# Performance work log

Hardware: AMD Instinct MI355X
Metric: run time of the kernel (lower is better)

Reference implementation:

```python
import jax, jax.numpy as jnp
import numpy as np

N_NODES = 50000
N_EDGES = 800000
IN_DIM = 64
EDGE_DIM = 16
HID = 128
L = 3
G = 128  # number of graphs in the batch
EPS = 1e-5


def _glorot(key, shape):
    fan_in, fan_out = shape[0], shape[1]
    lim = float(np.sqrt(6.0 / (fan_in + fan_out)))
    return jax.random.uniform(key, shape, jnp.float32, -lim, lim)


def setup_inputs() -> dict:
    key = jax.random.key(0)
    ks = jax.random.split(key, 40)
    inp = {}
    inp["x"] = jax.random.uniform(ks[0], (N_NODES, IN_DIM), jnp.float32)
    inp["edge_index"] = jax.random.randint(ks[1], (2, N_EDGES), 0, N_NODES, jnp.int64)
    inp["edge_attr"] = jax.random.normal(ks[2], (N_EDGES, EDGE_DIM), jnp.float32)
    inp["batch"] = jnp.sort(jax.random.randint(ks[3], (N_NODES,), 0, G, jnp.int64))
    # ligand / protein input MLPs: Linear-ReLU-Linear-ReLU
    inp["lig_w1"] = _glorot(ks[4], (IN_DIM, HID)); inp["lig_b1"] = jnp.zeros((HID,), jnp.float32)
    inp["lig_w2"] = _glorot(ks[5], (HID, HID));    inp["lig_b2"] = jnp.zeros((HID,), jnp.float32)
    inp["prot_w1"] = _glorot(ks[6], (IN_DIM, HID)); inp["prot_b1"] = jnp.zeros((HID,), jnp.float32)
    inp["prot_w2"] = _glorot(ks[7], (HID, HID));    inp["prot_b2"] = jnp.zeros((HID,), jnp.float32)
    # per-layer GINEConv params (stacked over layers)
    inp["edge_w"] = jnp.stack([_glorot(ks[8 + i], (EDGE_DIM, HID)) for i in range(L)])
    inp["edge_b"] = jnp.zeros((L, HID), jnp.float32)
    inp["nn_w1"] = jnp.stack([_glorot(ks[12 + i], (HID, HID)) for i in range(L)])
    inp["nn_b1"] = jnp.zeros((L, HID), jnp.float32)
    inp["nn_w2"] = jnp.stack([_glorot(ks[16 + i], (HID, HID)) for i in range(L)])
    inp["nn_b2"] = jnp.zeros((L, HID), jnp.float32)
    # GraphNorm params: weight=1, bias=0, mean_scale=1
    inp["gn_w"] = jnp.ones((L, HID), jnp.float32)
    inp["gn_b"] = jnp.zeros((L, HID), jnp.float32)
    inp["gn_ms"] = jnp.ones((L, HID), jnp.float32)
    # output head: Linear-ReLU-Linear(1)
    inp["fc_w1"] = _glorot(ks[20], (HID, HID)); inp["fc_b1"] = jnp.zeros((HID,), jnp.float32)
    inp["fc_w2"] = _glorot(ks[21], (HID, 1));   inp["fc_b2"] = jnp.zeros((1,), jnp.float32)
    return inp


def reference(x, edge_index, edge_attr, batch,
              lig_w1, lig_b1, lig_w2, lig_b2,
              prot_w1, prot_b1, prot_w2, prot_b2,
              edge_w, edge_b, nn_w1, nn_b1, nn_w2, nn_b2,
              gn_w, gn_b, gn_ms,
              fc_w1, fc_b1, fc_w2, fc_b2):
    relu = lambda a: jnp.maximum(a, 0)
    src, dst = edge_index[0], edge_index[1]

    # input encoders, merged per node by protein flag (last feature column)
    is_prot = x[:, -1] > 0.5
    h_lig = relu(relu(x @ lig_w1 + lig_b1) @ lig_w2 + lig_b2)
    h_prot = relu(relu(x @ prot_w1 + prot_b1) @ prot_w2 + prot_b2)
    h = jnp.where(is_prot[:, None], h_prot, h_lig)

    # per-graph node counts for GraphNorm
    cnt = jax.ops.segment_sum(jnp.ones((x.shape[0],), jnp.float32), batch, num_segments=G)
    cnt = jnp.maximum(cnt, 1.0)[:, None]

    for l in range(L):
        # GINEConv (eps=0): out = nn(x + sum_{j->i} relu(x_j + lin(e_ji)))
        e = edge_attr @ edge_w[l] + edge_b[l]              # [E, HID]
        msg = relu(h[src] + e)                             # gather + add + relu
        aggr = jax.ops.segment_sum(msg, dst, num_segments=h.shape[0])
        h = aggr + h
        h = relu(h @ nn_w1[l] + nn_b1[l]) @ nn_w2[l] + nn_b2[l]
        # GraphNorm: per-graph mean/var with learnable mean_scale
        mean = jax.ops.segment_sum(h, batch, num_segments=G) / cnt
        hc = h - mean[batch] * gn_ms[l]
        var = jax.ops.segment_sum(hc * hc, batch, num_segments=G) / cnt
        h = gn_w[l] * hc * jax.lax.rsqrt(var[batch] + EPS) + gn_b[l]
        h = relu(h)  # (dropout=0.0 -> identity)

    g = jax.ops.segment_sum(h, batch, num_segments=G)      # global_add_pool
    out = relu(g @ fc_w1 + fc_b1) @ fc_w2 + fc_b2
    return out.reshape(-1)
```

## Files before the change

kernel.cpp:

```cpp
#include <hip/hip_runtime.h>

#define N_NODES 50000
#define N_EDGES 800000
#define IN_DIM  64
#define EDGE_DIM 16
#define HID     128
#define NLAYERS 3
#define NGRAPH  128
#define EPS     1e-5f

typedef __attribute__((ext_vector_type(8))) short bf8_t;
typedef __attribute__((ext_vector_type(4))) float f32x4;

__device__ __forceinline__ unsigned short f2bf(float x) {
    unsigned u = __float_as_uint(x);
    unsigned r = u + 0x7fffu + ((u >> 16) & 1u);
    return (unsigned short)(r >> 16);
}
__device__ __forceinline__ float bf2f(unsigned short v) {
    return __uint_as_float(((unsigned)v) << 16);
}

__global__ void k_init(int* __restrict__ row_cnt, float* __restrict__ pool,
                       float* __restrict__ gsum, float* __restrict__ gsq) {
    int i = blockIdx.x * blockDim.x + threadIdx.x;
    if (i < N_NODES) row_cnt[i] = 0;
    if (i < NGRAPH * HID) { pool[i] = 0.0f; gsum[i] = 0.0f; gsq[i] = 0.0f; }
}

__global__ __launch_bounds__(NGRAPH) void k_count(const int* __restrict__ batch,
                                                  float* __restrict__ cnt) {
    int g = threadIdx.x;
    int lo = 0, hi = N_NODES;
    while (lo < hi) { int mid = (lo + hi) >> 1; if (batch[mid] < g) lo = mid + 1; else hi = mid; }
    int a = lo;
    lo = 0; hi = N_NODES;
    while (lo < hi) { int mid = (lo + hi) >> 1; if (batch[mid] < g + 1) lo = mid + 1; else hi = mid; }
    cnt[g] = (float)(lo - a);
}

__global__ void k_wconv(const float* __restrict__ nw1, const float* __restrict__ nw2,
                        unsigned short* __restrict__ wt) {
    int idx = blockIdx.x * 256 + threadIdx.x;
    if (idx >= NLAYERS * 2 * HID * HID) return;
    int k = idx & 127;
    int n = (idx >> 7) & 127;
    int which = (idx >> 14) & 1;
    int l = idx >> 15;
    const float* w = (which == 0 ? nw1 : nw2) + l * HID * HID;
    wt[idx] = f2bf(w[k * HID + n]);
}

__global__ void k_wconv_enc(const float* __restrict__ lw1, const float* __restrict__ pw1,
                            const float* __restrict__ lw2, const float* __restrict__ pw2,
                            unsigned short* __restrict__ we) {
    int idx = blockIdx.x * 256 + threadIdx.x;
    if (idx >= 49152) return;
    float v;
    if (idx < 8192)       { int n = idx >> 6, k = idx & 63;            v = lw1[k * HID + n]; }
    else if (idx < 16384) { int r = idx - 8192;  int n = r >> 6, k = r & 63;  v = pw1[k * HID + n]; }
    else if (idx < 32768) { int r = idx - 16384; int n = r >> 7, k = r & 127; v = lw2[k * HID + n]; }
    else                  { int r = idx - 32768; int n = r >> 7, k = r & 127; v = pw2[k * HID + n]; }
    we[idx] = f2bf(v);
}

__global__ void k_wconv_e(const float* __restrict__ ew, unsigned short* __restrict__ wte) {
    int idx = blockIdx.x * 256 + threadIdx.x;
    if (idx >= NLAYERS * 8 * 64 * 8) return;
    int j = idx & 7;
    int lane = (idx >> 3) & 63;
    int t = (idx >> 9) & 7;
    int l = idx >> 12;
    int k = (lane >> 4) * 8 + j;
    int feat = t * 16 + (lane & 15);
    float v = (k < EDGE_DIM) ? ew[l * EDGE_DIM * HID + k * HID + feat] : 0.0f;
    wte[idx] = f2bf(v);
}

__global__ void k_hist(const int* __restrict__ dsts, int* __restrict__ row_cnt) {
    int e = blockIdx.x * blockDim.x + threadIdx.x;
    if (e < N_EDGES) atomicAdd(&row_cnt[dsts[e]], 1);
}

__global__ __launch_bounds__(256) void k_scan1(const int* __restrict__ row_cnt,
                                               int* __restrict__ partial) {
    __shared__ int s[256];
    int t = threadIdx.x, b = blockIdx.x;
    int i0 = b * 512 + t;
    int v = 0;
    if (i0 < N_NODES) v += row_cnt[i0];
    if (i0 + 256 < N_NODES) v += row_cnt[i0 + 256];
    s[t] = v; __syncthreads();
    for (int off = 128; off > 0; off >>= 1) {
        if (t < off) s[t] += s[t + off];
        __syncthreads();
    }
    if (t == 0) partial[b] = s[0];
}

#define NCHUNK 98
__global__ __launch_bounds__(128) void k_scan2(int* __restrict__ partial) {
    __shared__ int s[128];
    int t = threadIdx.x;
    int v = (t < NCHUNK) ? partial[t] : 0;
    s[t] = v; __syncthreads();
    for (int off = 1; off < 128; off <<= 1) {
        int x = (t >= off) ? s[t - off] : 0;
        __syncthreads();
        s[t] += x;
        __syncthreads();
    }
    partial[t] = s[t] - v;
}

__global__ __launch_bounds__(512) void k_scan3(const int* __restrict__ row_cnt,
                                               const int* __restrict__ partial,
                                               int* __restrict__ row_start,
                                               int* __restrict__ row_fill) {
    __shared__ int s[512];
    int t = threadIdx.x, b = blockIdx.x;
    int i = b * 512 + t;
    int v = (i < N_NODES) ? row_cnt[i] : 0;
    s[t] = v; __syncthreads();
    for (int off = 1; off < 512; off <<= 1) {
        int x = (t >= off) ? s[t - off] : 0;
        __syncthreads();
        s[t] += x;
        __syncthreads();
    }
    int excl = s[t] - v + partial[b];
    if (i < N_NODES) { row_start[i] = excl; row_fill[i] = excl; }
}

__global__ void k_fill(const int* __restrict__ srcs, const int* __restrict__ dsts,
                       const float* __restrict__ ea,
                       int* __restrict__ row_fill,
                       int* __restrict__ csr_src, unsigned short* __restrict__ cea) {
    int e = blockIdx.x * blockDim.x + threadIdx.x;
    if (e < N_EDGES) {
        int p = atomicAdd(&row_fill[dsts[e]], 1);
        csr_src[p] = srcs[e];
        const float* s = ea + (size_t)e * EDGE_DIM;
        bf8_t v0, v1;
        #pragma unroll
        for (int k = 0; k < 8; ++k) v0[k] = (short)f2bf(s[k]);
        #pragma unroll
        for (int k = 0; k < 8; ++k) v1[k] = (short)f2bf(s[8 + k]);
        *(bf8_t*)(cea + (size_t)p * EDGE_DIM) = v0;
        *(bf8_t*)(cea + (size_t)p * EDGE_DIM + 8) = v1;
    }
}

#define HS 136
__global__ __launch_bounds__(256) void k_encoder_mfma(
    const float* __restrict__ x,
    const unsigned short* __restrict__ we,
    const float* __restrict__ lb1, const float* __restrict__ lb2,
    const float* __restrict__ pb1, const float* __restrict__ pb2,
    unsigned short* __restrict__ Hbp) {
    __shared__ short h1l[4 * 16 * HS];
    __shared__ short h1p[4 * 16 * HS];
    int w = threadIdx.x >> 6, lane = threadIdx.x & 63;
    int m = lane & 15, quad = lane >> 4;
    int nb = blockIdx.x * 64 + w * 16;
    short* hl = h1l + w * 16 * HS;
    short* hp = h1p + w * 16 * HS;
    int nclamp = nb + m; if (nclamp >= N_NODES) nclamp = N_NODES - 1;
    const float* xp = x + (size_t)nclamp * IN_DIM;

    f32x4 a1l[8], a1p[8];
    #pragma unroll
    for (int t = 0; t < 8; ++t) {
        float bl = lb1[t * 16 + m], bp = pb1[t * 16 + m];
        a1l[t] = (f32x4){bl, bl, bl, bl};
        a1p[t] = (f32x4){bp, bp, bp, bp};
    }
    #pragma unroll
    for (int s_ = 0; s_ < 2; ++s_) {
        int k0 = s_ * 32 + quad * 8;
        float4 a0 = *(const float4*)(xp + k0);
        float4 a1v = *(const float4*)(xp + k0 + 4);
        bf8_t af;
        af[0] = (short)f2bf(a0.x); af[1] = (short)f2bf(a0.y);
        af[2] = (short)f2bf(a0.z); af[3] = (short)f2bf(a0.w);
        af[4] = (short)f2bf(a1v.x); af[5] = (short)f2bf(a1v.y);
        af[6] = (short)f2bf(a1v.z); af[7] = (short)f2bf(a1v.w);
        #pragma unroll
        for (int t = 0; t < 8; ++t) {
            bf8_t bl = *(const bf8_t*)(we + (t * 16 + m) * 64 + k0);
            bf8_t bp = *(const bf8_t*)(we + 8192 + (t * 16 + m) * 64 + k0);
            a1l[t] = __builtin_amdgcn_mfma_f32_16x16x32_bf16(af, bl, a1l[t], 0, 0, 0);
            a1p[t] = __builtin_amdgcn_mfma_f32_16x16x32_bf16(af, bp, a1p[t], 0, 0, 0);
        }
    }
    #pragma unroll
    for (int t = 0; t < 8; ++t)
        #pragma unroll
        for (int r = 0; r < 4; ++r) {
            hl[(quad * 4 + r) * HS + t * 16 + m] = (short)f2bf(fmaxf(a1l[t][r], 0.0f));
            hp[(quad * 4 + r) * HS + t * 16 + m] = (short)f2bf(fmaxf(a1p[t][r], 0.0f));
        }
    __syncthreads();
    f32x4 a2l[8], a2p[8];
    #pragma unroll
    for (int t = 0; t < 8; ++t) {
        float bl = lb2[t * 16 + m], bp = pb2[t * 16 + m];
        a2l[t] = (f32x4){bl, bl, bl, bl};
        a2p[t] = (f32x4){bp, bp, bp, bp};
    }
    #pragma unroll
    for (int s_ = 0; s_ < 4; ++s_) {
        int k0 = s_ * 32 + quad * 8;
        bf8_t afl = *(const bf8_t*)(hl + m * HS + k0);
        bf8_t afp = *(const bf8_t*)(hp + m * HS + k0);
        #pragma unroll
        for (int t = 0; t < 8; ++t) {
            bf8_t bl = *(const bf8_t*)(we + 16384 + (t * 16 + m) * 128 + k0);
            bf8_t bp = *(const bf8_t*)(we + 32768 + (t * 16 + m) * 128 + k0);
            a2l[t] = __builtin_amdgcn_mfma_f32_16x16x32_bf16(afl, bl, a2l[t], 0, 0, 0);
            a2p[t] = __builtin_amdgcn_mfma_f32_16x16x32_bf16(afp, bp, a2p[t], 0, 0, 0);
        }
    }
    #pragma unroll
    for (int r = 0; r < 4; ++r) {
        int node = nb + quad * 4 + r;
        if (node < N_NODES) {
            float flg = x[(size_t)node * IN_DIM + (IN_DIM - 1)];
            bool prot = flg > 0.5f;
            bf8_t o;
            #pragma unroll
            for (int t = 0; t < 8; ++t) {
                float v = prot ? a2p[t][r] : a2l[t][r];
                o[t] = (short)f2bf(fmaxf(v, 0.0f));
            }
            *(bf8_t*)(Hbp + (size_t)node * HID + m * 8) = o;
        }
    }
}

__global__ __launch_bounds__(256) void k_gather(
    const int* __restrict__ csr_src, const unsigned short* __restrict__ cea,
    const int* __restrict__ row_start, const int* __restrict__ row_end,
    const unsigned short* __restrict__ wte, const float* __restrict__ eb,
    const unsigned short* __restrict__ Hbp, float* __restrict__ A) {
    int w = threadIdx.x >> 6, lane = threadIdx.x & 63;
    int m = lane & 15, quad = lane >> 4;
    int n = blockIdx.x * 4 + w;
    bf8_t bw[8];
    #pragma unroll
    for (int t = 0; t < 8; ++t)
        bw[t] = *(const bf8_t*)(wte + ((size_t)t * 64 + lane) * 8);
    float ebv[8];
    #pragma unroll
    for (int t = 0; t < 8; ++t) ebv[t] = eb[t * 16 + m];
    float acc[8];
    #pragma unroll
    for (int t = 0; t < 8; ++t) acc[t] = 0.0f;

    int p  = __builtin_amdgcn_readfirstlane(row_start[n]);
    int pe = __builtin_amdgcn_readfirstlane(row_end[n]);

    for (; p + 16 <= pe; p += 16) {
        bf8_t af = (bf8_t){0, 0, 0, 0, 0, 0, 0, 0};
        if (quad < 2)
            af = *(const bf8_t*)(cea + (size_t)(p + m) * EDGE_DIM + quad * 8);
        int sr[4];
        #pragma unroll
        for (int r = 0; r < 4; ++r) sr[r] = csr_src[p + quad * 4 + r];
        bf8_t hrow[4];
        #pragma unroll
        for (int r = 0; r < 4; ++r)
            hrow[r] = *(const bf8_t*)(Hbp + (size_t)sr[r] * HID + m * 8);
        f32x4 d[8];
        #pragma unroll
        for (int t = 0; t < 8; ++t)
            d[t] = __builtin_amdgcn_mfma_f32_16x16x32_bf16(
                af, bw[t], (f32x4){ebv[t], ebv[t], ebv[t], ebv[t]}, 0, 0, 0);
        #pragma unroll
        for (int t = 0; t < 8; ++t)
            #pragma unroll
            for (int r = 0; r < 4; ++r)
                acc[t] += fmaxf(bf2f((unsigned short)hrow[r][t]) + d[t][r], 0.0f);
    }
    int rem = pe - p;
    if (rem > 0) {
        bf8_t af = (bf8_t){0, 0, 0, 0, 0, 0, 0, 0};
        if (quad < 2 && m < rem)
            af = *(const bf8_t*)(cea + (size_t)(p + m) * EDGE_DIM + quad * 8);
        int sr[4];
        #pragma unroll
        for (int r = 0; r < 4; ++r) {
            int idx = p + quad * 4 + r; if (idx >= pe) idx = pe - 1;
            sr[r] = csr_src[idx];
        }
        bf8_t hrow[4];
        #pragma unroll
        for (int r = 0; r < 4; ++r)
            hrow[r] = *(const bf8_t*)(Hbp + (size_t)sr[r] * HID + m * 8);
        f32x4 d[8];
        #pragma unroll
        for (int t = 0; t < 8; ++t)
            d[t] = __builtin_amdgcn_mfma_f32_16x16x32_bf16(
                af, bw[t], (f32x4){ebv[t], ebv[t], ebv[t], ebv[t]}, 0, 0, 0);
        #pragma unroll
        for (int t = 0; t < 8; ++t)
            #pragma unroll
            for (int r = 0; r < 4; ++r)
                if (quad * 4 + r < rem)
                    acc[t] += fmaxf(bf2f((unsigned short)hrow[r][t]) + d[t][r], 0.0f);
    }
    #pragma unroll
    for (int t = 0; t < 8; ++t) {
        acc[t] += __shfl_xor(acc[t], 16);
        acc[t] += __shfl_xor(acc[t], 32);
    }
    int t0 = quad * 2, t1 = quad * 2 + 1;
    const unsigned short* selfp = Hbp + (size_t)n * HID + m * 8;
    float s0 = bf2f(selfp[t0]);
    float s1 = bf2f(selfp[t1]);
    size_t base = (size_t)n * HID;
    A[base + t0 * 16 + m] = acc[t0] + s0;
    A[base + t1 * 16 + m] = acc[t1] + s1;
}

#define MLP_NODES_PER_BLOCK 64
__global__ __launch_bounds__(256) void k_mlp_mfma(
    const float* __restrict__ A, const int* __restrict__ batch,
    const unsigned short* __restrict__ wt1, const unsigned short* __restrict__ wt2,
    const float* __restrict__ b1, const float* __restrict__ b2,
    float* __restrict__ H, float* __restrict__ gsum, float* __restrict__ gsq) {
    __shared__ short h1s[4 * 16 * HS];
    int w = threadIdx.x >> 6;
    int lane = threadIdx.x & 63;
    int m = lane & 15;
    int quad = lane >> 4;
    int nb = blockIdx.x * MLP_NODES_PER_BLOCK + w * 16;
    short* hw = h1s + w * 16 * HS;

    int nclamp = nb + m; if (nclamp >= N_NODES) nclamp = N_NODES - 1;
    const float* Ap = A + (size_t)nclamp * HID;
    f32x4 acc1[8];
    #pragma unroll
    for (int t = 0; t < 8; ++t) {
        float bv = b1[t * 16 + m];
        acc1[t] = (f32x4){bv, bv, bv, bv};
    }
    #pragma unroll
    for (int s_ = 0; s_ < 4; ++s_) {
        int k0 = s_ * 32 + quad * 8;
        float4 a0 = *(const float4*)(Ap + k0);
        float4 a1 = *(const float4*)(Ap + k0 + 4);
        bf8_t af;
        af[0] = (short)f2bf(a0.x); af[1] = (short)f2bf(a0.y);
        af[2] = (short)f2bf(a0.z); af[3] = (short)f2bf(a0.w);
        af[4] = (short)f2bf(a1.x); af[5] = (short)f2bf(a1.y);
        af[6] = (short)f2bf(a1.z); af[7] = (short)f2bf(a1.w);
        #pragma unroll
        for (int t = 0; t < 8; ++t) {
            bf8_t bf = *(const bf8_t*)(wt1 + (t * 16 + m) * HID + k0);
            acc1[t] = __builtin_amdgcn_mfma_f32_16x16x32_bf16(af, bf, acc1[t], 0, 0, 0);
        }
    }
    #pragma unroll
    for (int t = 0; t < 8; ++t)
        #pragma unroll
        for (int r = 0; r < 4; ++r) {
            float v = fmaxf(acc1[t][r], 0.0f);
            hw[(quad * 4 + r) * HS + t * 16 + m] = (short)f2bf(v);
        }
    __syncthreads();
    f32x4 acc2[8];
    #pragma unroll
    for (int t = 0; t < 8; ++t) {
        float bv = b2[t * 16 + m];
        acc2[t] = (f32x4){bv, bv, bv, bv};
    }
    #pragma unroll
    for (int s_ = 0; s_ < 4; ++s_) {
        int k0 = s_ * 32 + quad * 8;
        bf8_t af = *(const bf8_t*)(hw + m * HS + k0);
        #pragma unroll
        for (int t = 0; t < 8; ++t) {
            bf8_t bf = *(const bf8_t*)(wt2 + (t * 16 + m) * HID + k0);
            acc2[t] = __builtin_amdgcn_mfma_f32_16x16x32_bf16(af, bf, acc2[t], 0, 0, 0);
        }
    }
    #pragma unroll
    for (int t = 0; t < 8; ++t)
        #pragma unroll
        for (int r = 0; r < 4; ++r) {
            int node = nb + quad * 4 + r;
            if (node < N_NODES) H[(size_t)node * HID + t * 16 + m] = acc2[t][r];
        }
    int blast = nb + 15 < N_NODES ? batch[nb + 15] : -1;
    int g0 = batch[nb < N_NODES ? nb : N_NODES - 1];
    if (nb + 15 < N_NODES && g0 == blast) {
        #pragma unroll
        for (int t = 0; t < 8; ++t) {
            float s = 0.0f, q = 0.0f;
            #pragma unroll
            for (int r = 0; r < 4; ++r) { float v = acc2[t][r]; s += v; q += v * v; }
            s += __shfl_xor(s, 16); q += __shfl_xor(q, 16);
            s += __shfl_xor(s, 32); q += __shfl_xor(q, 32);
            if (quad == 0) {
                atomicAdd(&gsum[g0 * HID + t * 16 + m], s);
                atomicAdd(&gsq[g0 * HID + t * 16 + m], q);
            }
        }
    } else {
        #pragma unroll
        for (int t = 0; t < 8; ++t)
            #pragma unroll
            for (int r = 0; r < 4; ++r) {
                int node = nb + quad * 4 + r;
                if (node < N_NODES) {
                    int g = batch[node];
                    float v = acc2[t][r];
                    atomicAdd(&gsum[g * HID + t * 16 + m], v);
                    atomicAdd(&gsq[g * HID + t * 16 + m], v * v);
                }
            }
    }
}

__global__ __launch_bounds__(HID) void k_stats(
    float* __restrict__ gsum, float* __restrict__ gsq,
    const float* __restrict__ cnt,
    const float* __restrict__ gw, const float* __restrict__ gb,
    const float* __restrict__ gms,
    float* __restrict__ sc, float* __restrict__ of) {
    int g = blockIdx.x;
    int t = threadIdx.x;
    float c = fmaxf(cnt[g], 1.0f);
    float mean = gsum[g * HID + t] / c;
    float msq  = gsq[g * HID + t] / c;
    float ms = gms[t];
    float var = msq - mean * mean * ms * (2.0f - ms);
    var = fmaxf(var, 0.0f);
    float istd = rsqrtf(var + EPS);
    float s = gw[t] * istd;
    sc[g * HID + t] = s;
    of[g * HID + t] = gb[t] - s * mean * ms;
    gsum[g * HID + t] = 0.0f;
    gsq[g * HID + t]  = 0.0f;
}

#define NORM_N 8
__global__ __launch_bounds__(HID) void k_norm(
    const float* __restrict__ H, const int* __restrict__ batch,
    const float* __restrict__ sc, const float* __restrict__ of,
    unsigned short* __restrict__ Hbp, float* __restrict__ pool, int accumulate) {
    int n0 = blockIdx.x * NORM_N;
    int t = threadIdx.x;
    int m = t & 15, tt = t >> 4;
    int g0 = batch[n0], gN = batch[n0 + NORM_N - 1];
    if (g0 == gN) {
        float ssc = sc[g0 * HID + t], sof = of[g0 * HID + t];
        float ps = 0.0f;
        #pragma unroll
        for (int i = 0; i < NORM_N; ++i) {
            float v = fmaxf(H[(size_t)(n0 + i) * HID + t] * ssc + sof, 0.0f);
            Hbp[(size_t)(n0 + i) * HID + m * 8 + tt] = f2bf(v);
            ps += v;
        }
        if (accumulate) atomicAdd(&pool[g0 * HID + t], ps);
    } else {
        #pragma unroll
        for (int i = 0; i < NORM_N; ++i) {
            int g = batch[n0 + i];
            float v = fmaxf(H[(size_t)(n0 + i) * HID + t] * sc[g * HID + t] + of[g * HID + t], 0.0f);
            Hbp[(size_t)(n0 + i) * HID + m * 8 + tt] = f2bf(v);
            if (accumulate) atomicAdd(&pool[g * HID + t], v);
        }
    }
}

__global__ __launch_bounds__(HID) void k_head(
    const float* __restrict__ pool,
    const float* __restrict__ fw1, const float* __restrict__ fb1,
    const float* __restrict__ fw2, const float* __restrict__ fb2,
    float* __restrict__ out) {
    __shared__ float ps[HID];
    __shared__ float red[2];
    int g = blockIdx.x;
    int t = threadIdx.x;
    ps[t] = pool[g * HID + t];
    __syncthreads();
    float acc = fb1[t];
    #pragma unroll 4
    for (int k = 0; k < HID; ++k) acc = fmaf(ps[k], fw1[k * HID + t], acc);
    float p = fmaxf(acc, 0.0f) * fw2[t];
    #pragma unroll
    for (int off = 32; off > 0; off >>= 1) p += __shfl_down(p, off, 64);
    if ((t & 63) == 0) red[t >> 6] = p;
    __syncthreads();
    if (t == 0) out[g] = red[0] + red[1] + fb2[0];
}

extern "C" void kernel_launch(void* const* d_in, const int* in_sizes, int n_in,
                              void* d_out, int out_size, void* d_ws, size_t ws_size,
                              hipStream_t stream) {
    const float* x     = (const float*)d_in[0];
    const int*   ei    = (const int*)d_in[1];
    const float* ea    = (const float*)d_in[2];
    const int*   batch = (const int*)d_in[3];
    const float* lw1 = (const float*)d_in[4];
    const float* lb1 = (const float*)d_in[5];
    const float* lw2 = (const float*)d_in[6];
    const float* lb2 = (const float*)d_in[7];
    const float* pw1 = (const float*)d_in[8];
    const float* pb1 = (const float*)d_in[9];
    const float* pw2 = (const float*)d_in[10];
    const float* pb2 = (const float*)d_in[11];
    const float* ew  = (const float*)d_in[12];
    const float* eb  = (const float*)d_in[13];
    const float* nw1 = (const float*)d_in[14];
    const float* nb1 = (const float*)d_in[15];
    const float* nw2 = (const float*)d_in[16];
    const float* nb2 = (const float*)d_in[17];
    const float* gw  = (const float*)d_in[18];
    const float* gb  = (const float*)d_in[19];
    const float* gms = (const float*)d_in[20];
    const float* fw1 = (const float*)d_in[21];
    const float* fb1 = (const float*)d_in[22];
    const float* fw2 = (const float*)d_in[23];
    const float* fb2 = (const float*)d_in[24];
    float* out = (float*)d_out;

    float* ws   = (float*)d_ws;
    float* H    = ws;
    float* A    = H    + (size_t)N_NODES * HID;
    float* gsum = A    + (size_t)N_NODES * HID;
    float* gsq  = gsum + NGRAPH * HID;
    float* sc   = gsq  + NGRAPH * HID;
    float* of   = sc   + NGRAPH * HID;
    float* pool = of   + NGRAPH * HID;
    float* cnt  = pool + NGRAPH * HID;
    int* row_cnt   = (int*)(cnt + NGRAPH);
    int* row_start = row_cnt + N_NODES;
    int* row_fill  = row_start + N_NODES;
    int* partial   = row_fill + N_NODES;
    int* csr_src   = partial + 128;
    unsigned short* cea  = (unsigned short*)(csr_src + N_EDGES);
    unsigned short* wt   = cea + (size_t)N_EDGES * EDGE_DIM;
    unsigned short* wenc = wt + NLAYERS * 2 * HID * HID;
    unsigned short* wte  = wenc + 49152;
    unsigned short* Hbp  = wte + NLAYERS * 8 * 64 * 8;

    const int* srcs = ei;
    const int* dsts = ei + N_EDGES;

    k_init<<<(N_NODES + 255) / 256, 256, 0, stream>>>(row_cnt, pool, gsum, gsq);
    k_count<<<1, NGRAPH, 0, stream>>>(batch, cnt);
    k_wconv<<<(NLAYERS * 2 * HID * HID + 255) / 256, 256, 0, stream>>>(nw1, nw2, wt);
    k_wconv_enc<<<(49152 + 255) / 256, 256, 0, stream>>>(lw1, pw1, lw2, pw2, wenc);
    k_wconv_e<<<(NLAYERS * 8 * 64 * 8 + 255) / 256, 256, 0, stream>>>(ew, wte);
    k_hist<<<(N_EDGES + 255) / 256, 256, 0, stream>>>(dsts, row_cnt);
    k_scan1<<<NCHUNK, 256, 0, stream>>>(row_cnt, partial);
    k_scan2<<<1, 128, 0, stream>>>(partial);
    k_scan3<<<NCHUNK, 512, 0, stream>>>(row_cnt, partial, row_start, row_fill);
    k_fill<<<(N_EDGES + 255) / 256, 256, 0, stream>>>(srcs, dsts, ea, row_fill,
                                                      csr_src, cea);

    k_encoder_mfma<<<(N_NODES + 63) / 64, 256, 0, stream>>>(
        x, wenc, lb1, lb2, pb1, pb2, Hbp);

    int mlp_blocks = (N_NODES + MLP_NODES_PER_BLOCK - 1) / MLP_NODES_PER_BLOCK;
    for (int l = 0; l < NLAYERS; ++l) {
        k_gather<<<N_NODES / 4, 256, 0, stream>>>(
            csr_src, cea, row_start, row_fill,
            wte + (size_t)l * 4096, eb + l * HID, Hbp, A);
        k_mlp_mfma<<<mlp_blocks, 256, 0, stream>>>(
            A, batch,
            wt + (size_t)l * 2 * HID * HID,
            wt + (size_t)l * 2 * HID * HID + HID * HID,
            nb1 + l * HID, nb2 + l * HID, H, gsum, gsq);
        k_stats<<<NGRAPH, HID, 0, stream>>>(gsum, gsq, cnt,
                                            gw + l * HID, gb + l * HID, gms + l * HID,
                                            sc, of);
        k_norm<<<N_NODES / NORM_N, HID, 0, stream>>>(
            H, batch, sc, of, Hbp, pool, (l == NLAYERS - 1) ? 1 : 0);
    }
    k_head<<<NGRAPH, HID, 0, stream>>>(pool, fw1, fb1, fw2, fb2, out);
}
```

Measured before the change: 707.1 us.

## Store gather output in bf16 and process eight nodes per wave

The gather kernel now writes the aggregated node features as bf16 instead of fp32, so k_mlp_mfma loads bf16 directly and no longer converts per element. That halves the traffic for the intermediate A buffer. Each wave now loops over eight destination nodes, which amortises the loads of the edge-weight fragments and biases and cuts the block count. The unpacking of the H rows was also rewritten as bit ops on uint4 words. The cost is fewer resident waves and less parallelism per node, plus one extra rounding of the aggregate to bf16, although the MLP previously rounded it to bf16 anyway.

```diff
diff --git a/kernel.cpp b/kernel.cpp
--- a/kernel.cpp
+++ b/kernel.cpp
@@ -238,14 +238,15 @@
     }
 }
 
+#define NPW 8
 __global__ __launch_bounds__(256) void k_gather(
     const int* __restrict__ csr_src, const unsigned short* __restrict__ cea,
     const int* __restrict__ row_start, const int* __restrict__ row_end,
     const unsigned short* __restrict__ wte, const float* __restrict__ eb,
-    const unsigned short* __restrict__ Hbp, float* __restrict__ A) {
+    const unsigned short* __restrict__ Hbp, unsigned short* __restrict__ Abp) {
     int w = threadIdx.x >> 6, lane = threadIdx.x & 63;
     int m = lane & 15, quad = lane >> 4;
-    int n = blockIdx.x * 4 + w;
+    int n0 = (blockIdx.x * 4 + w) * NPW;
     bf8_t bw[8];
     #pragma unroll
     for (int t = 0; t < 8; ++t)
@@ -253,79 +254,102 @@
     float ebv[8];
     #pragma unroll
     for (int t = 0; t < 8; ++t) ebv[t] = eb[t * 16 + m];
-    float acc[8];
-    #pragma unroll
-    for (int t = 0; t < 8; ++t) acc[t] = 0.0f;
-
-    int p  = __builtin_amdgcn_readfirstlane(row_start[n]);
-    int pe = __builtin_amdgcn_readfirstlane(row_end[n]);
-
-    for (; p + 16 <= pe; p += 16) {
-        bf8_t af = (bf8_t){0, 0, 0, 0, 0, 0, 0, 0};
-        if (quad < 2)
-            af = *(const bf8_t*)(cea + (size_t)(p + m) * EDGE_DIM + quad * 8);
-        int sr[4];
-        #pragma unroll
-        for (int r = 0; r < 4; ++r) sr[r] = csr_src[p + quad * 4 + r];
-        bf8_t hrow[4];
-        #pragma unroll
-        for (int r = 0; r < 4; ++r)
-            hrow[r] = *(const bf8_t*)(Hbp + (size_t)sr[r] * HID + m * 8);
-        f32x4 d[8];
-        #pragma unroll
-        for (int t = 0; t < 8; ++t)
-            d[t] = __builtin_amdgcn_mfma_f32_16x16x32_bf16(
-                af, bw[t], (f32x4){ebv[t], ebv[t], ebv[t], ebv[t]}, 0, 0, 0);
-        #pragma unroll
-        for (int t = 0; t < 8; ++t)
+
+    for (int ni = 0; ni < NPW; ++ni) {
+        int n = n0 + ni;
+        if (n >= N_NODES) break;
+        float2 accp[4];
+        #pragma unroll
+        for (int i = 0; i < 4; ++i) accp[i] = make_float2(0.0f, 0.0f);
+
+        int p  = __builtin_amdgcn_readfirstlane(row_start[n]);
+        int pe = __builtin_amdgcn_readfirstlane(row_end[n]);
+
+        for (; p + 16 <= pe; p += 16) {
+            bf8_t af = (bf8_t){0, 0, 0, 0, 0, 0, 0, 0};
+            if (quad < 2)
+                af = *(const bf8_t*)(cea + (size_t)(p + m) * EDGE_DIM + quad * 8);
+            int sr[4];
+            #pragma unroll
+            for (int r = 0; r < 4; ++r) sr[r] = csr_src[p + quad * 4 + r];
+            uint4 hu[4];
             #pragma unroll
             for (int r = 0; r < 4; ++r)
-                acc[t] += fmaxf(bf2f((unsigned short)hrow[r][t]) + d[t][r], 0.0f);
-    }
-    int rem = pe - p;
-    if (rem > 0) {
-        bf8_t af = (bf8_t){0, 0, 0, 0, 0, 0, 0, 0};
-        if (quad < 2 && m < rem)
-            af = *(const bf8_t*)(cea + (size_t)(p + m) * EDGE_DIM + quad * 8);
-        int sr[4];
-        #pragma unroll
-        for (int r = 0; r < 4; ++r) {
-            int idx = p + quad * 4 + r; if (idx >= pe) idx = pe - 1;
-            sr[r] = csr_src[idx];
-        }
-        bf8_t hrow[4];
-        #pragma unroll
-        for (int r = 0; r < 4; ++r)
-            hrow[r] = *(const bf8_t*)(Hbp + (size_t)sr[r] * HID + m * 8);
-        f32x4 d[8];
-        #pragma unroll
-        for (int t = 0; t < 8; ++t)
-            d[t] = __builtin_amdgcn_mfma_f32_16x16x32_bf16(
-                af, bw[t], (f32x4){ebv[t], ebv[t], ebv[t], ebv[t]}, 0, 0, 0);
-        #pragma unroll
-        for (int t = 0; t < 8; ++t)
+                hu[r] = *(const uint4*)(Hbp + (size_t)sr[r] * HID + m * 8);
+            f32x4 d[8];
+            #pragma unroll
+            for (int t = 0; t < 8; ++t)
+                d[t] = __builtin_amdgcn_mfma_f32_16x16x32_bf16(
+                    af, bw[t], (f32x4){ebv[t], ebv[t], ebv[t], ebv[t]}, 0, 0, 0);
+            #pragma unroll
+            for (int r = 0; r < 4; ++r) {
+                const unsigned* hw_ = (const unsigned*)&hu[r];
+                #pragma unroll
+                for (int i = 0; i < 4; ++i) {
+                    unsigned u = hw_[i];
+                    float2 hv = make_float2(__uint_as_float(u << 16),
+                                            __uint_as_float(u & 0xffff0000u));
+                    float2 sv = make_float2(hv.x + d[2 * i][r], hv.y + d[2 * i + 1][r]);
+                    accp[i].x += fmaxf(sv.x, 0.0f);
+                    accp[i].y += fmaxf(sv.y, 0.0f);
+                }
+            }
+        }
+        int rem = pe - p;
+        if (rem > 0) {
+            bf8_t af = (bf8_t){0, 0, 0, 0, 0, 0, 0, 0};
+            if (quad < 2 && m < rem)
+                af = *(const bf8_t*)(cea + (size_t)(p + m) * EDGE_DIM + quad * 8);
+            int sr[4];
+            #pragma unroll
+            for (int r = 0; r < 4; ++r) {
+                int idx = p + quad * 4 + r; if (idx >= pe) idx = pe - 1;
+                sr[r] = csr_src[idx];
+            }
+            uint4 hu[4];
             #pragma unroll
             for (int r = 0; r < 4; ++r)
-                if (quad * 4 + r < rem)
-                    acc[t] += fmaxf(bf2f((unsigned short)hrow[r][t]) + d[t][r], 0.0f);
-    }
-    #pragma unroll
-    for (int t = 0; t < 8; ++t) {
-        acc[t] += __shfl_xor(acc[t], 16);
-        acc[t] += __shfl_xor(acc[t], 32);
-    }
-    int t0 = quad * 2, t1 = quad * 2 + 1;
-    const unsigned short* selfp = Hbp + (size_t)n * HID + m * 8;
-    float s0 = bf2f(selfp[t0]);
-    float s1 = bf2f(selfp[t1]);
-    size_t base = (size_t)n * HID;
-    A[base + t0 * 16 + m] = acc[t0] + s0;
-    A[base + t1 * 16 + m] = acc[t1] + s1;
+                hu[r] = *(const uint4*)(Hbp + (size_t)sr[r] * HID + m * 8);
+            f32x4 d[8];
+            #pragma unroll
+            for (int t = 0; t < 8; ++t)
+                d[t] = __builtin_amdgcn_mfma_f32_16x16x32_bf16(
+                    af, bw[t], (f32x4){ebv[t], ebv[t], ebv[t], ebv[t]}, 0, 0, 0);
+            #pragma unroll
+            for (int r = 0; r < 4; ++r) {
+                if (quad * 4 + r >= rem) continue;
+                const unsigned* hw_ = (const unsigned*)&hu[r];
+                #pragma unroll
+                for (int i = 0; i < 4; ++i) {
+                    unsigned u = hw_[i];
+                    float2 hv = make_float2(__uint_as_float(u << 16),
+                                            __uint_as_float(u & 0xffff0000u));
+                    float2 sv = make_float2(hv.x + d[2 * i][r], hv.y + d[2 * i + 1][r]);
+                    accp[i].x += fmaxf(sv.x, 0.0f);
+                    accp[i].y += fmaxf(sv.y, 0.0f);
+                }
+            }
+        }
+        #pragma unroll
+        for (int i = 0; i < 4; ++i) {
+            accp[i].x += __shfl_xor(accp[i].x, 16);
+            accp[i].y += __shfl_xor(accp[i].y, 16);
+            accp[i].x += __shfl_xor(accp[i].x, 32);
+            accp[i].y += __shfl_xor(accp[i].y, 32);
+        }
+        int t0 = quad * 2, t1 = quad * 2 + 1;
+        const unsigned short* selfp = Hbp + (size_t)n * HID + m * 8;
+        float s0 = bf2f(selfp[t0]);
+        float s1 = bf2f(selfp[t1]);
+        size_t base = (size_t)n * HID;
+        Abp[base + t0 * 16 + m] = f2bf(accp[quad].x + s0);
+        Abp[base + t1 * 16 + m] = f2bf(accp[quad].y + s1);
+    }
 }
 
 #define MLP_NODES_PER_BLOCK 64
 __global__ __launch_bounds__(256) void k_mlp_mfma(
-    const float* __restrict__ A, const int* __restrict__ batch,
+    const unsigned short* __restrict__ Abp, const int* __restrict__ batch,
     const unsigned short* __restrict__ wt1, const unsigned short* __restrict__ wt2,
     const float* __restrict__ b1, const float* __restrict__ b2,
     float* __restrict__ H, float* __restrict__ gsum, float* __restrict__ gsq) {
@@ -338,7 +362,7 @@
     short* hw = h1s + w * 16 * HS;
 
     int nclamp = nb + m; if (nclamp >= N_NODES) nclamp = N_NODES - 1;
-    const float* Ap = A + (size_t)nclamp * HID;
+    const unsigned short* Ap = Abp + (size_t)nclamp * HID;
     f32x4 acc1[8];
     #pragma unroll
     for (int t = 0; t < 8; ++t) {
@@ -348,13 +372,7 @@
     #pragma unroll
     for (int s_ = 0; s_ < 4; ++s_) {
         int k0 = s_ * 32 + quad * 8;
-        float4 a0 = *(const float4*)(Ap + k0);
-        float4 a1 = *(const float4*)(Ap + k0 + 4);
-        bf8_t af;
-        af[0] = (short)f2bf(a0.x); af[1] = (short)f2bf(a0.y);
-        af[2] = (short)f2bf(a0.z); af[3] = (short)f2bf(a0.w);
-        af[4] = (short)f2bf(a1.x); af[5] = (short)f2bf(a1.y);
-        af[6] = (short)f2bf(a1.z); af[7] = (short)f2bf(a1.w);
+        bf8_t af = *(const bf8_t*)(Ap + k0);
         #pragma unroll
         for (int t = 0; t < 8; ++t) {
             bf8_t bf = *(const bf8_t*)(wt1 + (t * 16 + m) * HID + k0);
@@ -546,6 +564,7 @@
     unsigned short* wenc = wt + NLAYERS * 2 * HID * HID;
     unsigned short* wte  = wenc + 49152;
     unsigned short* Hbp  = wte + NLAYERS * 8 * 64 * 8;
+    unsigned short* Abp  = (unsigned short*)A;
 
     const int* srcs = ei;
     const int* dsts = ei + N_EDGES;
@@ -565,13 +584,14 @@
     k_encoder_mfma<<<(N_NODES + 63) / 64, 256, 0, stream>>>(
         x, wenc, lb1, lb2, pb1, pb2, Hbp);
 
+    int gat_blocks = (N_NODES + 4 * NPW - 1) / (4 * NPW);
     int mlp_blocks = (N_NODES + MLP_NODES_PER_BLOCK - 1) / MLP_NODES_PER_BLOCK;
     for (int l = 0; l < NLAYERS; ++l) {
-        k_gather<<<N_NODES / 4, 256, 0, stream>>>(
+        k_gather<<<gat_blocks, 256, 0, stream>>>(
             csr_src, cea, row_start, row_fill,
-            wte + (size_t)l * 4096, eb + l * HID, Hbp, A);
+            wte + (size_t)l * 4096, eb + l * HID, Hbp, Abp);
         k_mlp_mfma<<<mlp_blocks, 256, 0, stream>>>(
-            A, batch,
+            Abp, batch,
             wt + (size_t)l * 2 * HID * HID,
             wt + (size_t)l * 2 * HID * HID + HID * HID,
             nb1 + l * HID, nb2 + l * HID, H, gsum, gsq);
```

New measurement: 779.5 us. +10.2%, slower.
